# Performance work log

Measured on AMD Instinct MI355X. Metric: run time of the kernel, lower is better.

The kernel has to match this reference:

```python
import jax, jax.numpy as jnp
import numpy as np

LEADER_IDX = 0
SOCIAL_DIST = 1.5
COHESION = 0.8
B, N, T = 64, 64, 100


def setup_inputs() -> dict:
    key = jax.random.key(0)
    k1, k2, k3, k4, k5 = jax.random.split(key, 5)
    # trajectories: (x, y, vel, yaw, acc, yawvel)
    x = jax.random.normal(k1, (B, N, T, 6), dtype=jnp.float32) * 5.0
    # world_from_agent: per-agent SE(2) homogeneous transform (B, 3, 3)
    theta = jax.random.uniform(k2, (B,), minval=-np.pi, maxval=np.pi)
    c, s = jnp.cos(theta), jnp.sin(theta)
    trans = jax.random.normal(k3, (B, 2), dtype=jnp.float32) * 50.0
    wfa = (jnp.zeros((B, 3, 3), dtype=jnp.float32)
           .at[:, 0, 0].set(c).at[:, 0, 1].set(-s)
           .at[:, 1, 0].set(s).at[:, 1, 1].set(c)
           .at[:, :2, 2].set(trans).at[:, 2, 2].set(1.0))
    # externalized randomness of torch forward (randint over B-1 choices, rand<p)
    rand_idx = jax.random.randint(k4, (T * N, B), 0, B - 1, dtype=jnp.int32)
    drop_mask = jax.random.uniform(k5, (T * N, B)) < COHESION
    return {"x": x, "world_from_agent": wfa, "rand_idx": rand_idx, "drop_mask": drop_mask}


def reference(x, world_from_agent, rand_idx, drop_mask):
    pos = x[..., :2]                                   # (B, N, T, 2)
    R = world_from_agent[:, :2, :2]                    # (B, 2, 2)
    t = world_from_agent[:, :2, 2]                     # (B, 2)
    pos_g = jnp.einsum('bntj,bij->bnti', pos, R) + t[:, None, None, :]
    # leader positions are detached (no grad), but same value in fwd
    leader = (jnp.arange(B) == LEADER_IDX)[:, None, None, None]
    pos_g = jnp.where(leader, jax.lax.stop_gradient(pos_g), pos_g)
    # (B,N,T,2) -> (T,N,B,2) -> (T*N, B, 2)  (matches torch transpose(0,2).reshape)
    flat = jnp.transpose(pos_g, (2, 1, 0, 3)).reshape(T * N, B, 2)
    # pairwise euclidean distances via norm trick (avoids (TN,B,B,2) diff tensor)
    sq = jnp.sum(flat * flat, axis=-1)                 # (TN, B)
    d2 = sq[:, :, None] + sq[:, None, :] - 2.0 * jnp.einsum('tbd,tcd->tbc', flat, flat)
    dist = jnp.sqrt(jnp.maximum(d2, 1e-12))            # (TN, B, B)
    eye = jnp.eye(B, dtype=bool)
    dist = jnp.where(eye[None], jnp.inf, dist)         # mask self-distance
    min_nb = jnp.argmin(dist, axis=-1).astype(jnp.int32)      # (TN, B)
    # row b of neighbor_choices is [0..b-1, b+1..B-1]; gather at rand_idx ->
    # value = rand_idx + (rand_idx >= b)
    b_idx = jnp.arange(B, dtype=jnp.int32)[None, :]
    rand_nb = rand_idx + (rand_idx >= b_idx).astype(jnp.int32)
    nb = jnp.where(drop_mask, rand_nb, min_nb)         # (TN, B)
    nd = jnp.take_along_axis(dist, nb[..., None], axis=2)[..., 0]  # (TN, B)
    nd = jnp.transpose(nd.reshape(T, N, B), (2, 1, 0))  # (B, N, T)
    loss = jnp.mean((nd - SOCIAL_DIST) ** 2, axis=-1)   # (B, N)
    return loss
```

## Files before the change

kernel.cpp:

```cpp
#include <hip/hip_runtime.h>

#define BB 64
#define NN 64
#define TT 100
#define S_TOT (NN * TT)
#define WAVES_PER_BLOCK 4

__device__ __forceinline__ float bcast(float v, int lane) {
    return __int_as_float(__builtin_amdgcn_readlane(__float_as_int(v), lane));
}

__global__ __launch_bounds__(256) void social_slice_kernel(
    const float* __restrict__ x,
    const float* __restrict__ wfa,
    const int* __restrict__ rand_idx,
    const int* __restrict__ drop_mask,
    float* __restrict__ ws)
{
    const int w = threadIdx.x >> 6;
    const int b = threadIdx.x & 63;
    const int s = blockIdx.x * WAVES_PER_BLOCK + w;
    const int t = s >> 6;
    const int n = s & 63;

    const float* wp = wfa + b * 9;
    const float r00 = wp[0], r01 = wp[1], tx = wp[2];
    const float r10 = wp[3], r11 = wp[4], ty = wp[5];

    const size_t xoff = (((size_t)b * NN + n) * (size_t)TT + (size_t)t) * 6;
    const float2 p = *(const float2*)(x + xoff);

    const float gx = r00 * p.x + r01 * p.y + tx;
    const float gy = r10 * p.x + r11 * p.y + ty;
    const float sq = gx * gx + gy * gy;

    float best = 3.4e38f;
    int besti = 0;
    #pragma unroll
    for (int c = 0; c < BB; ++c) {
        const float qx = bcast(gx, c);
        const float qy = bcast(gy, c);
        const float qz = bcast(sq, c);
        const float dot = fmaf(gx, qx, gy * qy);
        float d2 = fmaf(-2.0f, dot, sq + qz);
        d2 = fmaxf(d2, 1e-12f);
        const bool take = (c != b) && (d2 < best);
        best  = take ? d2 : best;
        besti = take ? c : besti;
    }

    const size_t sb = (size_t)s * BB + b;
    const int r = rand_idx[sb];
    const int rnb = r + (r >= b ? 1 : 0);
    const int nb = drop_mask[sb] ? rnb : besti;

    const float qx = __shfl(gx, nb);
    const float qy = __shfl(gy, nb);
    const float qz = __shfl(sq, nb);
    const float dot = fmaf(gx, qx, gy * qy);
    const float d2 = fmaxf(fmaf(-2.0f, dot, sq + qz), 1e-12f);
    const float nd = sqrtf(d2);
    const float diff = nd - 1.5f;

    ws[sb] = diff * diff;
}

__global__ __launch_bounds__(256) void social_reduce_kernel(
    const float* __restrict__ ws,
    float* __restrict__ out)
{
    const int b = threadIdx.x & 63;
    const int n = blockIdx.x * 4 + (threadIdx.x >> 6);

    float acc0 = 0.f, acc1 = 0.f, acc2 = 0.f, acc3 = 0.f;
    #pragma unroll 4
    for (int t = 0; t < TT; t += 4) {
        acc0 += ws[((t + 0) * NN + n) * BB + b];
        acc1 += ws[((t + 1) * NN + n) * BB + b];
        acc2 += ws[((t + 2) * NN + n) * BB + b];
        acc3 += ws[((t + 3) * NN + n) * BB + b];
    }
    out[b * NN + n] = ((acc0 + acc1) + (acc2 + acc3)) * (1.0f / TT);
}

extern "C" void kernel_launch(void* const* d_in, const int* in_sizes, int n_in,
                              void* d_out, int out_size, void* d_ws, size_t ws_size,
                              hipStream_t stream) {
    const float* x = (const float*)d_in[0];
    const float* wfa = (const float*)d_in[1];
    const int* rand_idx = (const int*)d_in[2];
    const int* drop_mask = (const int*)d_in[3];
    float* out = (float*)d_out;
    float* ws = (float*)d_ws;

    social_slice_kernel<<<S_TOT / WAVES_PER_BLOCK, 256, 0, stream>>>(
        x, wfa, rand_idx, drop_mask, ws);
    social_reduce_kernel<<<NN / 4, 256, 0, stream>>>(ws, out);
}
```

Measured before the change: 78.97 us.

## Group four timesteps per block, stage loads in LDS, pre-reduce before workspace

Each block now handles one agent n and four consecutive timesteps. Positions are loaded with four adjacent t values per agent, so those reads land close together in memory, and they are staged in shared memory. The block sums the four per-timestep squared errors in LDS before writing, which cuts the workspace writes and the second kernel's reads by four. The argmin loop is split into four independent accumulator chains for more ILP, and the rand_idx and drop_mask loads are issued early. This adds two block barriers and a merge step whose tie-breaking must keep the lowest index.

```diff
diff --git a/kernel.cpp b/kernel.cpp
--- a/kernel.cpp
+++ b/kernel.cpp
@@ -3,8 +3,8 @@
 #define BB 64
 #define NN 64
 #define TT 100
-#define S_TOT (NN * TT)
-#define WAVES_PER_BLOCK 4
+#define TQ 4
+#define NTQ (TT / TQ)
 
 __device__ __forceinline__ float bcast(float v, int lane) {
     return __int_as_float(__builtin_amdgcn_readlane(__float_as_int(v), lane));
@@ -17,52 +17,98 @@
     const int* __restrict__ drop_mask,
     float* __restrict__ ws)
 {
+    const int n  = blockIdx.x & 63;
+    const int tq = blockIdx.x >> 6;
+    const int t0 = tq * TQ;
+
+    __shared__ float2 S[TQ][BB + 1];
+    __shared__ float  Rld[TQ][BB];
+
+    {
+        const int lb = threadIdx.x >> 2;
+        const int k  = threadIdx.x & 3;
+        const float* wp = wfa + lb * 9;
+        const float r00 = wp[0], r01 = wp[1], tx = wp[2];
+        const float r10 = wp[3], r11 = wp[4], ty = wp[5];
+        const size_t xoff = (((size_t)lb * NN + n) * (size_t)TT + (size_t)(t0 + k)) * 6;
+        const float2 p = *(const float2*)(x + xoff);
+        const float gx = r00 * p.x + r01 * p.y + tx;
+        const float gy = r10 * p.x + r11 * p.y + ty;
+        S[k][lb] = make_float2(gx, gy);
+    }
+    __syncthreads();
+
     const int w = threadIdx.x >> 6;
     const int b = threadIdx.x & 63;
-    const int s = blockIdx.x * WAVES_PER_BLOCK + w;
-    const int t = s >> 6;
-    const int n = s & 63;
+    const int t = t0 + w;
+    const int s = t * NN + n;
+    const size_t sb = (size_t)s * BB + b;
+    const int r  = rand_idx[sb];
+    const int dm = drop_mask[sb];
 
-    const float* wp = wfa + b * 9;
-    const float r00 = wp[0], r01 = wp[1], tx = wp[2];
-    const float r10 = wp[3], r11 = wp[4], ty = wp[5];
-
-    const size_t xoff = (((size_t)b * NN + n) * (size_t)TT + (size_t)t) * 6;
-    const float2 p = *(const float2*)(x + xoff);
-
-    const float gx = r00 * p.x + r01 * p.y + tx;
-    const float gy = r10 * p.x + r11 * p.y + ty;
+    const float2 g = S[w][b];
+    const float gx = g.x, gy = g.y;
     const float sq = gx * gx + gy * gy;
 
-    float best = 3.4e38f;
-    int besti = 0;
+    float bd0 = 3.4e38f, bd1 = 3.4e38f, bd2 = 3.4e38f, bd3 = 3.4e38f;
+    int   bi0 = 0, bi1 = 16, bi2 = 32, bi3 = 48;
     #pragma unroll
-    for (int c = 0; c < BB; ++c) {
-        const float qx = bcast(gx, c);
-        const float qy = bcast(gy, c);
-        const float qz = bcast(sq, c);
-        const float dot = fmaf(gx, qx, gy * qy);
-        float d2 = fmaf(-2.0f, dot, sq + qz);
-        d2 = fmaxf(d2, 1e-12f);
-        const bool take = (c != b) && (d2 < best);
-        best  = take ? d2 : best;
-        besti = take ? c : besti;
+    for (int i = 0; i < 16; ++i) {
+        {
+            const int c = i;
+            const float qx = bcast(gx, c), qy = bcast(gy, c), qz = bcast(sq, c);
+            float d2 = fmaf(-2.0f, fmaf(gx, qx, gy * qy), sq + qz);
+            d2 = fmaxf(d2, 1e-12f);
+            const bool take = (c != b) && (d2 < bd0);
+            bd0 = take ? d2 : bd0;  bi0 = take ? c : bi0;
+        }
+        {
+            const int c = 16 + i;
+            const float qx = bcast(gx, c), qy = bcast(gy, c), qz = bcast(sq, c);
+            float d2 = fmaf(-2.0f, fmaf(gx, qx, gy * qy), sq + qz);
+            d2 = fmaxf(d2, 1e-12f);
+            const bool take = (c != b) && (d2 < bd1);
+            bd1 = take ? d2 : bd1;  bi1 = take ? c : bi1;
+        }
+        {
+            const int c = 32 + i;
+            const float qx = bcast(gx, c), qy = bcast(gy, c), qz = bcast(sq, c);
+            float d2 = fmaf(-2.0f, fmaf(gx, qx, gy * qy), sq + qz);
+            d2 = fmaxf(d2, 1e-12f);
+            const bool take = (c != b) && (d2 < bd2);
+            bd2 = take ? d2 : bd2;  bi2 = take ? c : bi2;
+        }
+        {
+            const int c = 48 + i;
+            const float qx = bcast(gx, c), qy = bcast(gy, c), qz = bcast(sq, c);
+            float d2 = fmaf(-2.0f, fmaf(gx, qx, gy * qy), sq + qz);
+            d2 = fmaxf(d2, 1e-12f);
+            const bool take = (c != b) && (d2 < bd3);
+            bd3 = take ? d2 : bd3;  bi3 = take ? c : bi3;
+        }
     }
+    float best = bd0; int besti = bi0;
+    if (bd1 < best) { best = bd1; besti = bi1; }
+    if (bd2 < best) { best = bd2; besti = bi2; }
+    if (bd3 < best) { best = bd3; besti = bi3; }
 
-    const size_t sb = (size_t)s * BB + b;
-    const int r = rand_idx[sb];
     const int rnb = r + (r >= b ? 1 : 0);
-    const int nb = drop_mask[sb] ? rnb : besti;
+    const int nb  = dm ? rnb : besti;
 
     const float qx = __shfl(gx, nb);
     const float qy = __shfl(gy, nb);
     const float qz = __shfl(sq, nb);
     const float dot = fmaf(gx, qx, gy * qy);
-    const float d2 = fmaxf(fmaf(-2.0f, dot, sq + qz), 1e-12f);
-    const float nd = sqrtf(d2);
+    const float d2m = fmaxf(fmaf(-2.0f, dot, sq + qz), 1e-12f);
+    const float nd = sqrtf(d2m);
     const float diff = nd - 1.5f;
+    Rld[w][b] = diff * diff;
+    __syncthreads();
 
-    ws[sb] = diff * diff;
+    if (w == 0) {
+        const float sum4 = ((Rld[0][b] + Rld[1][b]) + Rld[2][b]) + Rld[3][b];
+        ws[((size_t)tq * NN + n) * BB + b] = sum4;
+    }
 }
 
 __global__ __launch_bounds__(256) void social_reduce_kernel(
@@ -72,15 +118,11 @@
     const int b = threadIdx.x & 63;
     const int n = blockIdx.x * 4 + (threadIdx.x >> 6);
 
-    float acc0 = 0.f, acc1 = 0.f, acc2 = 0.f, acc3 = 0.f;
-    #pragma unroll 4
-    for (int t = 0; t < TT; t += 4) {
-        acc0 += ws[((t + 0) * NN + n) * BB + b];
-        acc1 += ws[((t + 1) * NN + n) * BB + b];
-        acc2 += ws[((t + 2) * NN + n) * BB + b];
-        acc3 += ws[((t + 3) * NN + n) * BB + b];
-    }
-    out[b * NN + n] = ((acc0 + acc1) + (acc2 + acc3)) * (1.0f / TT);
+    float acc = 0.f;
+    #pragma unroll
+    for (int tq = 0; tq < NTQ; ++tq)
+        acc += ws[((size_t)tq * NN + n) * BB + b];
+    out[b * NN + n] = acc * (1.0f / TT);
 }
 
 extern "C" void kernel_launch(void* const* d_in, const int* in_sizes, int n_in,
@@ -93,7 +135,7 @@
     float* out = (float*)d_out;
     float* ws = (float*)d_ws;
 
-    social_slice_kernel<<<S_TOT / WAVES_PER_BLOCK, 256, 0, stream>>>(
+    social_slice_kernel<<<NTQ * NN, 256, 0, stream>>>(
         x, wfa, rand_idx, drop_mask, ws);
     social_reduce_kernel<<<NN / 4, 256, 0, stream>>>(ws, out);
 }
```

Result: faster. 76.52 us (-3.1%).
